# Optimization experiments

Hardware: AMD Instinct MI355X
Metric: run time of the kernel (lower is better)

## Reference

```python
import jax, jax.numpy as jnp
import numpy as np
from itertools import product

S0 = 384          # voxel grid size per max_data_size
N0 = 500_000      # active surface voxels
NF_IN, NF = 2, 16
EPS = 1e-4        # scn.BatchNormReLU default eps


def _make_nbr(lin, S, offs):
    # submanifold rulebook: nbr[k, i] = row of active neighbor of site i at offset k, else sentinel N
    N = len(lin)
    x = lin // (S * S); y = (lin // S) % S; z = lin % S
    nbr = np.full((len(offs), N), N, np.int32)
    for k, (dx, dy, dz) in enumerate(offs):
        nx, ny, nz = x + dx, y + dy, z + dz
        valid = (nx >= 0) & (nx < S) & (ny >= 0) & (ny < S) & (nz >= 0) & (nz < S)
        q = (nx * S + ny) * S + nz
        pos = np.minimum(np.searchsorted(lin, q), N - 1)
        nbr[k] = np.where(valid & (lin[pos] == q), pos, N).astype(np.int32)
    return nbr


def _downsample(lin, S):
    # half-resolution active sites, unpool parent map, and 2x2x2 stride-2 conv rulebook
    x = lin // (S * S); y = (lin // S) % S; z = lin % S
    Sh = S // 2
    plin = ((x // 2) * Sh + (y // 2)) * Sh + (z // 2)
    lin_h = np.unique(plin)
    parent = np.searchsorted(lin_h, plin).astype(np.int32)
    xh = lin_h // (Sh * Sh); yh = (lin_h // Sh) % Sh; zh = lin_h % Sh
    N, Nh = len(lin), len(lin_h)
    down = np.full((8, Nh), N, np.int32)
    for k, (ox, oy, oz) in enumerate(product((0, 1), repeat=3)):
        q = ((2 * xh + ox) * S + (2 * yh + oy)) * S + (2 * zh + oz)
        pos = np.minimum(np.searchsorted(lin, q), N - 1)
        down[k] = np.where(lin[pos] == q, pos, N).astype(np.int32)
    return lin_h, parent, down


def setup_inputs() -> dict:
    rng = np.random.default_rng(0)
    cand = rng.integers(0, S0 ** 3, size=int(N0 * 1.1))
    lin0 = np.unique(cand)[:N0]
    assert len(lin0) == N0
    offs27 = list(product((-1, 0, 1), repeat=3))
    nbr0 = _make_nbr(lin0, S0, offs27)
    lin1, parent01, down01 = _downsample(lin0, S0)
    nbr1 = _make_nbr(lin1, S0 // 2, offs27)
    lin2, parent12, down12 = _downsample(lin1, S0 // 2)
    nbr2 = _make_nbr(lin2, S0 // 4, offs27)

    key = jax.random.key(0)
    ks = jax.random.split(key, 16)
    n = lambda k, sh, sc: jax.random.normal(k, sh, jnp.float32) * sc
    return dict(
        feats=n(ks[0], (N0, NF_IN), 1.0),
        w_p1=n(ks[1], (27, NF_IN, NF), 1.0 / np.sqrt(27 * NF_IN)),
        blk_bn1_g=1.0 + n(ks[2], (3, NF), 0.1), blk_bn1_b=n(ks[3], (3, NF), 0.1),
        blk_w1=n(ks[4], (3, 27, NF, NF), 1.0 / np.sqrt(27 * NF)),
        blk_bn2_g=1.0 + n(ks[5], (3, NF), 0.1), blk_bn2_b=n(ks[6], (3, NF), 0.1),
        blk_w2=n(ks[7], (3, 27, NF, NF), 1.0 / np.sqrt(27 * NF)),
        down_bn_g=1.0 + n(ks[8], (2, NF), 0.1), down_bn_b=n(ks[9], (2, NF), 0.1),
        down_w=n(ks[10], (2, 8, NF, NF), 1.0 / np.sqrt(8 * NF)),
        bn3_g=1.0 + n(ks[11], (3 * NF,), 0.1), bn3_b=n(ks[12], (3 * NF,), 0.1),
        w_sdf=n(ks[13], (3 * NF, 1), 1.0 / np.sqrt(3 * NF)),
        b_sdf=jnp.zeros((1,), jnp.float32),
        nbr0=jnp.asarray(nbr0), nbr1=jnp.asarray(nbr1), nbr2=jnp.asarray(nbr2),
        down01=jnp.asarray(down01), down12=jnp.asarray(down12),
        parent01=jnp.asarray(parent01), parent12=jnp.asarray(parent12),
    )


def _sconv(x, nbr, W):
    # rulebook gather-GEMM-accumulate sparse conv.
    # x: [Nin, Cin], nbr: [K, Nout] (index Nin == inactive sentinel), W: [K, Cin, Cout]
    xp = jnp.concatenate([x, jnp.zeros((1, x.shape[1]), x.dtype)], 0)
    acc0 = jnp.zeros((nbr.shape[1], W.shape[2]), x.dtype)
    def step(acc, kw):
        idx, Wk = kw
        return acc + xp[idx] @ Wk, None
    out, _ = jax.lax.scan(step, acc0, (nbr, W))
    return out


def _bnrelu(x, g, b):
    # SCN BatchNorm: batch stats over active sites only
    m = x.mean(0); v = x.var(0)
    return jax.nn.relu((x - m) * jax.lax.rsqrt(v + EPS) * g + b)


def _res_block(x, nbr, g1, b1, w1, g2, b2, w2):
    # pre-activation residual block, identity skip (in == out channels)
    h = _sconv(_bnrelu(x, g1, b1), nbr, w1)
    h = _sconv(_bnrelu(h, g2, b2), nbr, w2)
    return x + h


def reference(feats, w_p1, blk_bn1_g, blk_bn1_b, blk_w1, blk_bn2_g, blk_bn2_b,
              blk_w2, down_bn_g, down_bn_b, down_w, bn3_g, bn3_b, w_sdf, b_sdf,
              nbr0, nbr1, nbr2, down01, down12, parent01, parent12):
    blk = lambda x, nbr, i: _res_block(x, nbr, blk_bn1_g[i], blk_bn1_b[i], blk_w1[i],
                                       blk_bn2_g[i], blk_bn2_b[i], blk_w2[i])
    x = _sconv(feats, nbr0, w_p1)                                    # p1: submanifold conv nf_in->nf
    r0 = blk(x, nbr0, 0)                                             # FCN level 0 block
    y1 = _sconv(_bnrelu(r0, down_bn_g[0], down_bn_b[0]), down01, down_w[0])  # stride-2 conv
    r1 = blk(y1, nbr1, 1)                                            # level 1 block
    z2 = _sconv(_bnrelu(r1, down_bn_g[1], down_bn_b[1]), down12, down_w[1])
    r2 = blk(z2, nbr2, 2)                                            # level 2 block
    j1 = jnp.concatenate([r1, r2[parent12]], axis=-1)                # UnPool + JoinTable -> 2*nf
    j0 = jnp.concatenate([r0, j1[parent01]], axis=-1)                # UnPool + JoinTable -> 3*nf
    h = _bnrelu(j0, bn3_g, bn3_b)                                    # p3
    return h @ w_sdf + b_sdf                                         # sdf linear, [N0, 1]
```

## Files before the change

### kernel.cpp

```cpp
#include <hip/hip_runtime.h>

#define BN_EPS 1e-4f
#define NREP 8

typedef _Float16 f16x8 __attribute__((ext_vector_type(8)));
typedef _Float16 f16x4 __attribute__((ext_vector_type(4)));
typedef _Float16 f16x2 __attribute__((ext_vector_type(2)));
typedef float f32x4 __attribute__((ext_vector_type(4)));

__global__ __launch_bounds__(256) void tr_k(const int* __restrict__ nbr,
                                            int* __restrict__ nbrT,
                                            int N, int Nin)
{
    const int i = blockIdx.x * 256 + threadIdx.x;
    if (i >= N) return;
    int v[32];
#pragma unroll
    for (int k = 0; k < 27; ++k) v[k] = nbr[(size_t)k * N + i];
#pragma unroll
    for (int k = 27; k < 32; ++k) v[k] = Nin;
    int4* dst = (int4*)(nbrT + (size_t)i * 32);
#pragma unroll
    for (int j = 0; j < 8; ++j)
        dst[j] = make_int4(v[4 * j], v[4 * j + 1], v[4 * j + 2], v[4 * j + 3]);
}

__global__ __launch_bounds__(256, 4) void conv16t_k(
    const _Float16* __restrict__ A16,
    const int* __restrict__ nbrT,
    const _Float16* __restrict__ WB,
    float* __restrict__ out,
    float* __restrict__ stats_out,
    int Nout, int Nin, int addSkip)
{
    constexpr int K = 27, PAIRS = 14;
    __shared__ int lds[4][16 * 36];
    const int wave = threadIdx.x >> 6, lane = threadIdx.x & 63;
    const int l15 = lane & 15, q = lane >> 4;
    const int h = q & 1;
    const int th = q >> 1;
    int* L = lds[wave];

    f16x8 bfr[PAIRS];
#pragma unroll
    for (int p = 0; p < PAIRS; ++p)
        bfr[p] = *(const f16x8*)(WB + ((size_t)p * 64 + lane) * 8);

    const int ngroups = (Nout + 15) >> 4;
    float s = 0.f, ss = 0.f;

    for (int grp = blockIdx.x * 4 + wave; grp < ngroups; grp += gridDim.x * 4) {
        const int base = grp * 16;
        const int site = min(base + l15, Nout - 1);

        const int4* src = (const int4*)(nbrT + (size_t)site * 32);
        const int4 c0 = src[q];
        const int4 c1 = src[q + 4];
        *(int4*)(L + l15 * 36 + q * 4) = c0;
        *(int4*)(L + l15 * 36 + 16 + q * 4) = c1;

        int idxs[PAIRS];
#pragma unroll
        for (int p = 0; p < PAIRS; ++p) {
            const int t = 2 * p + ((2 * p + 1 < K) ? th : 0);
            idxs[p] = L[l15 * 36 + t];
        }

        f32x4 acc0 = {0.f, 0.f, 0.f, 0.f}, acc1 = {0.f, 0.f, 0.f, 0.f};
#pragma unroll
        for (int p = 0; p < PAIRS; ++p) {
            const int idx = idxs[p];
            if (__any(idx < Nin)) {
                f16x8 a = {};
                if (idx < Nin)
                    a = *(const f16x8*)(A16 + (size_t)idx * 16 + h * 8);
                if (p & 1) acc1 = __builtin_amdgcn_mfma_f32_16x16x32_f16(a, bfr[p], acc1, 0, 0, 0);
                else       acc0 = __builtin_amdgcn_mfma_f32_16x16x32_f16(a, bfr[p], acc0, 0, 0, 0);
            }
        }

#pragma unroll
        for (int r = 0; r < 4; ++r) {
            const int row = base + q * 4 + r;
            float v = acc0[r] + acc1[r];
            if (row < Nout) {
                float* op = out + (size_t)row * 16 + l15;
                if (addSkip) v += *op;
                *op = v;
                s += v; ss += v * v;
            }
        }
    }

    if (stats_out) {
        s  += __shfl_xor(s, 16);  s  += __shfl_xor(s, 32);
        ss += __shfl_xor(ss, 16); ss += __shfl_xor(ss, 32);
        __shared__ float red[4][32];
        if (lane < 16) { red[wave][l15] = s; red[wave][16 + l15] = ss; }
        __syncthreads();
        if (threadIdx.x < 32) {
            const int t2 = threadIdx.x;
            float* bank = stats_out + (blockIdx.x & (NREP - 1)) * 128;
            atomicAdd(bank + (t2 < 16 ? t2 : 48 + t2),
                      red[0][t2] + red[1][t2] + red[2][t2] + red[3][t2]);
        }
    }
}

template <int K>
__global__ __launch_bounds__(256, 4) void conv16_k(
    const _Float16* __restrict__ A16, const int* __restrict__ nbr,
    const _Float16* __restrict__ WB, float* __restrict__ out,
    float* __restrict__ stats_out, int Nout, int Nin, int addSkip)
{
    constexpr int PAIRS = (K + 1) / 2;
    const int wave = threadIdx.x >> 6, lane = threadIdx.x & 63;
    const int l15 = lane & 15, q = lane >> 4;
    const int h = q & 1, th = q >> 1;

    f16x8 bfr[PAIRS];
#pragma unroll
    for (int p = 0; p < PAIRS; ++p)
        bfr[p] = *(const f16x8*)(WB + ((size_t)p * 64 + lane) * 8);

    const int ngroups = (Nout + 15) >> 4;
    float s = 0.f, ss = 0.f;

    for (int grp = blockIdx.x * 4 + wave; grp < ngroups; grp += gridDim.x * 4) {
        const int base = grp * 16;
        const int site = min(base + l15, Nout - 1);
        f32x4 acc0 = {0.f, 0.f, 0.f, 0.f}, acc1 = {0.f, 0.f, 0.f, 0.f};
#pragma unroll
        for (int p = 0; p < PAIRS; ++p) {
            const int t = 2 * p + ((2 * p + 1 < K) ? th : 0);
            const int idx = nbr[(size_t)t * Nout + site];
            f16x8 a = {};
            if (idx < Nin)
                a = *(const f16x8*)(A16 + (size_t)idx * 16 + h * 8);
            if (p & 1) acc1 = __builtin_amdgcn_mfma_f32_16x16x32_f16(a, bfr[p], acc1, 0, 0, 0);
            else       acc0 = __builtin_amdgcn_mfma_f32_16x16x32_f16(a, bfr[p], acc0, 0, 0, 0);
        }
#pragma unroll
        for (int r = 0; r < 4; ++r) {
            const int row = base + q * 4 + r;
            float v = acc0[r] + acc1[r];
            if (row < Nout) {
                float* op = out + (size_t)row * 16 + l15;
                if (addSkip) v += *op;
                *op = v;
                s += v; ss += v * v;
            }
        }
    }

    if (stats_out) {
        s  += __shfl_xor(s, 16);  s  += __shfl_xor(s, 32);
        ss += __shfl_xor(ss, 16); ss += __shfl_xor(ss, 32);
        __shared__ float red[4][32];
        if (lane < 16) { red[wave][l15] = s; red[wave][16 + l15] = ss; }
        __syncthreads();
        if (threadIdx.x < 32) {
            const int t2 = threadIdx.x;
            float* bank = stats_out + (blockIdx.x & (NREP - 1)) * 128;
            atomicAdd(bank + (t2 < 16 ? t2 : 48 + t2),
                      red[0][t2] + red[1][t2] + red[2][t2] + red[3][t2]);
        }
    }
}

__global__ __launch_bounds__(256, 4) void convp1t_k(
    const _Float16* __restrict__ F16,
    const int* __restrict__ nbrT,
    const _Float16* __restrict__ WB,
    float* __restrict__ out, float* __restrict__ stats_out, int Nout)
{
    __shared__ int lds[4][16 * 36];
    const int wave = threadIdx.x >> 6, lane = threadIdx.x & 63;
    const int l15 = lane & 15, q = lane >> 4;
    int* L = lds[wave];

    f16x8 b0 = *(const f16x8*)(WB + (size_t)lane * 8);
    f16x8 b1 = *(const f16x8*)(WB + ((size_t)64 + lane) * 8);

    const int ngroups = (Nout + 15) >> 4;
    float s = 0.f, ss = 0.f;

    for (int grp = blockIdx.x * 4 + wave; grp < ngroups; grp += gridDim.x * 4) {
        const int base = grp * 16;
        const int site = min(base + l15, Nout - 1);

        const int4* src = (const int4*)(nbrT + (size_t)site * 32);
        const int4 c0 = src[q];
        const int4 c1 = src[q + 4];
        *(int4*)(L + l15 * 36 + q * 4) = c0;
        *(int4*)(L + l15 * 36 + 16 + q * 4) = c1;

        f32x4 acc = {0.f, 0.f, 0.f, 0.f};
#pragma unroll
        for (int mf = 0; mf < 2; ++mf) {
            int tid[4];
#pragma unroll
            for (int jt = 0; jt < 4; ++jt)
                tid[jt] = L[l15 * 36 + mf * 16 + q * 4 + jt];
            f16x8 a;
#pragma unroll
            for (int jt = 0; jt < 4; ++jt) {
                const int idx = tid[jt];
                f16x2 f = {};
                if (idx < Nout)
                    f = *(const f16x2*)(F16 + (size_t)idx * 2);
                a[jt * 2] = f.x; a[jt * 2 + 1] = f.y;
            }
            acc = __builtin_amdgcn_mfma_f32_16x16x32_f16(a, mf ? b1 : b0, acc, 0, 0, 0);
        }
#pragma unroll
        for (int r = 0; r < 4; ++r) {
            const int row = base + q * 4 + r;
            const float v = acc[r];
            if (row < Nout) {
                out[(size_t)row * 16 + l15] = v;
                s += v; ss += v * v;
            }
        }
    }

    s  += __shfl_xor(s, 16);  s  += __shfl_xor(s, 32);
    ss += __shfl_xor(ss, 16); ss += __shfl_xor(ss, 32);
    __shared__ float red[4][32];
    if (lane < 16) { red[wave][l15] = s; red[wave][16 + l15] = ss; }
    __syncthreads();
    if (threadIdx.x < 32) {
        const int t2 = threadIdx.x;
        float* bank = stats_out + (blockIdx.x & (NREP - 1)) * 128;
        atomicAdd(bank + (t2 < 16 ? t2 : 48 + t2),
                  red[0][t2] + red[1][t2] + red[2][t2] + red[3][t2]);
    }
}

__global__ void pack_k(const float* __restrict__ w_p1, const float* __restrict__ w1,
                       const float* __restrict__ w2, const float* __restrict__ dw,
                       _Float16* __restrict__ WBp1, _Float16* __restrict__ WB27,
                       _Float16* __restrict__ WB8)
{
    const int b = blockIdx.x;
    if (b == 0) {
        for (int v = threadIdx.x; v < 2 * 64 * 8; v += 256) {
            const int mf = v >> 9, lane = (v >> 3) & 63, j = v & 7;
            const int qq = lane >> 4, n = lane & 15;
            const int kg = mf * 32 + qq * 8 + j;
            const int t = kg >> 1, cin = kg & 1;
            WBp1[v] = (t < 27) ? (_Float16)w_p1[t * 32 + cin * 16 + n] : (_Float16)0.f;
        }
    } else if (b <= 6) {
        const int ti = b - 1, lvl = ti >> 1;
        const float* src = ((ti & 1) ? w2 : w1) + lvl * 6912;
        _Float16* dst = WB27 + (size_t)ti * (14 * 64 * 8);
        for (int v = threadIdx.x; v < 14 * 64 * 8; v += 256) {
            const int p = v >> 9, lane = (v >> 3) & 63, j = v & 7;
            const int qq = lane >> 4, n = lane & 15;
            const int t = 2 * p + (qq >> 1);
            const int cin = (qq & 1) * 8 + j;
            dst[v] = (t < 27) ? (_Float16)src[t * 256 + cin * 16 + n] : (_Float16)0.f;
        }
    } else {
        const int ti = b - 7;
        const float* src = dw + ti * 2048;
        _Float16* dst = WB8 + (size_t)ti * (4 * 64 * 8);
        for (int v = threadIdx.x; v < 4 * 64 * 8; v += 256) {
            const int p = v >> 9, lane = (v >> 3) & 63, j = v & 7;
            const int qq = lane >> 4, n = lane & 15;
            const int t = 2 * p + (qq >> 1);
            const int cin = (qq & 1) * 8 + j;
            dst[v] = (_Float16)src[t * 256 + cin * 16 + n];
        }
    }
}

__global__ __launch_bounds__(256) void apply16_k(
    const float* __restrict__ x, const float* __restrict__ stats,
    const float* __restrict__ g, const float* __restrict__ b,
    _Float16* __restrict__ A16, int N, float invN)
{
    const int t = blockIdx.x * 256 + threadIdx.x;
    if (t >= (N + 1) * 4) return;
    const int n = t >> 2, c = (t & 3) * 4;
    f16x4 r;
    if (n == N) {
        r[0] = r[1] = r[2] = r[3] = (_Float16)0.f;
    } else {
        const float4 v = *(const float4*)(x + (size_t)n * 16 + c);
        float vv[4] = {v.x, v.y, v.z, v.w};
#pragma unroll
        for (int i = 0; i < 4; ++i) {
            float su = 0.f, sq = 0.f;
#pragma unroll
            for (int rep = 0; rep < NREP; ++rep) {
                su += stats[rep * 128 + c + i];
                sq += stats[rep * 128 + 64 + c + i];
            }
            const float mean = su * invN;
            const float var  = sq * invN - mean * mean;
            const float sc   = g[c + i] * rsqrtf(var + BN_EPS);
            const float bi   = fmaf(-mean, sc, b[c + i]);
            r[i] = (_Float16)fmaxf(fmaf(vv[i], sc, bi), 0.f);
        }
    }
    *(f16x4*)(A16 + (size_t)n * 16 + c) = r;
}

__global__ void f16cvt_k(const float* __restrict__ f, _Float16* __restrict__ F16, int N)
{
    const int t = blockIdx.x * 256 + threadIdx.x;
    if (t > N) return;
    f16x2 r;
    if (t == N) { r[0] = r[1] = (_Float16)0.f; }
    else { const float2 v = *(const float2*)(f + (size_t)t * 2); r[0] = (_Float16)v.x; r[1] = (_Float16)v.y; }
    *(f16x2*)(F16 + (size_t)t * 2) = r;
}

__global__ void fin_k(float* __restrict__ stats, const float* __restrict__ g,
                      const float* __restrict__ b, float* __restrict__ sb,
                      int C, float invN)
{
    const int c = threadIdx.x;
    if (c < C) {
        float su = 0.f, sq = 0.f;
#pragma unroll
        for (int rep = 0; rep < NREP; ++rep) {
            su += stats[rep * 128 + c];
            sq += stats[rep * 128 + 64 + c];
        }
        const float mean = su * invN;
        const float var = sq * invN - mean * mean;
        const float s = g[c] * rsqrtf(var + BN_EPS);
        sb[c] = s;
        sb[64 + c] = fmaf(-mean, s, b[c]);
    }
}

__device__ __forceinline__ float wred(float v) {
#pragma unroll
    for (int off = 32; off > 0; off >>= 1) v += __shfl_xor(v, off);
    return v;
}

__global__ __launch_bounds__(256) void gstats_k(
    const float* __restrict__ R0, const float* __restrict__ R1,
    const float* __restrict__ R2, const int* __restrict__ p01,
    const int* __restrict__ p12, float* __restrict__ stats, int N0)
{
    float s[48], q[48];
#pragma unroll
    for (int c = 0; c < 48; ++c) { s[c] = 0.f; q[c] = 0.f; }

    for (int n = blockIdx.x * blockDim.x + threadIdx.x; n < N0;
         n += gridDim.x * blockDim.x) {
        const int i1 = p01[n];
        const int i2 = p12[i1];
        const float4* a0 = (const float4*)(R0 + (size_t)n * 16);
        const float4* a1 = (const float4*)(R1 + (size_t)i1 * 16);
        const float4* a2 = (const float4*)(R2 + (size_t)i2 * 16);
#pragma unroll
        for (int j = 0; j < 4; ++j) {
            const float4 v = a0[j]; const int c = 4 * j;
            s[c] += v.x; q[c] += v.x * v.x; s[c+1] += v.y; q[c+1] += v.y * v.y;
            s[c+2] += v.z; q[c+2] += v.z * v.z; s[c+3] += v.w; q[c+3] += v.w * v.w;
        }
#pragma unroll
        for (int j = 0; j < 4; ++j) {
            const float4 v = a1[j]; const int c = 16 + 4 * j;
            s[c] += v.x; q[c] += v.x * v.x; s[c+1] += v.y; q[c+1] += v.y * v.y;
            s[c+2] += v.z; q[c+2] += v.z * v.z; s[c+3] += v.w; q[c+3] += v.w * v.w;
        }
#pragma unroll
        for (int j = 0; j < 4; ++j) {
            const float4 v = a2[j]; const int c = 32 + 4 * j;
            s[c] += v.x; q[c] += v.x * v.x; s[c+1] += v.y; q[c+1] += v.y * v.y;
            s[c+2] += v.z; q[c+2] += v.z * v.z; s[c+3] += v.w; q[c+3] += v.w * v.w;
        }
    }

    __shared__ float red[4][96];
    const int wave = threadIdx.x >> 6, lane = threadIdx.x & 63;
#pragma unroll
    for (int c = 0; c < 48; ++c) {
        const float ss = wred(s[c]);
        const float qq = wred(q[c]);
        if (lane == 0) { red[wave][c] = ss; red[wave][48 + c] = qq; }
    }
    __syncthreads();
    const int t = threadIdx.x;
    if (t < 96) {
        float* bank = stats + (blockIdx.x & (NREP - 1)) * 128;
        const float v = red[0][t] + red[1][t] + red[2][t] + red[3][t];
        atomicAdd(bank + (t < 48 ? t : 64 + (t - 48)), v);
    }
}

__global__ __launch_bounds__(256) void out_k(
    const float* __restrict__ R0, const float* __restrict__ R1,
    const float* __restrict__ R2, const int* __restrict__ p01,
    const int* __restrict__ p12, const float* __restrict__ sb,
    const float* __restrict__ wsdf, const float* __restrict__ bsdf,
    float* __restrict__ out, int N0)
{
    const int n = blockIdx.x * 256 + threadIdx.x;
    if (n >= N0) return;
    const int i1 = p01[n];
    const int i2 = p12[i1];
    float acc = bsdf[0];
    const float4* a0 = (const float4*)(R0 + (size_t)n * 16);
    const float4* a1 = (const float4*)(R1 + (size_t)i1 * 16);
    const float4* a2 = (const float4*)(R2 + (size_t)i2 * 16);
#pragma unroll
    for (int j = 0; j < 4; ++j) {
        const float4 v = a0[j]; const int c = 4 * j;
        acc += fmaxf(fmaf(v.x, sb[c+0], sb[64+c+0]), 0.f) * wsdf[c+0];
        acc += fmaxf(fmaf(v.y, sb[c+1], sb[64+c+1]), 0.f) * wsdf[c+1];
        acc += fmaxf(fmaf(v.z, sb[c+2], sb[64+c+2]), 0.f) * wsdf[c+2];
        acc += fmaxf(fmaf(v.w, sb[c+3], sb[64+c+3]), 0.f) * wsdf[c+3];
    }
#pragma unroll
    for (int j = 0; j < 4; ++j) {
        const float4 v = a1[j]; const int c = 16 + 4 * j;
        acc += fmaxf(fmaf(v.x, sb[c+0], sb[64+c+0]), 0.f) * wsdf[c+0];
        acc += fmaxf(fmaf(v.y, sb[c+1], sb[64+c+1]), 0.f) * wsdf[c+1];
        acc += fmaxf(fmaf(v.z, sb[c+2], sb[64+c+2]), 0.f) * wsdf[c+2];
        acc += fmaxf(fmaf(v.w, sb[c+3], sb[64+c+3]), 0.f) * wsdf[c+3];
    }
#pragma unroll
    for (int j = 0; j < 4; ++j) {
        const float4 v = a2[j]; const int c = 32 + 4 * j;
        acc += fmaxf(fmaf(v.x, sb[c+0], sb[64+c+0]), 0.f) * wsdf[c+0];
        acc += fmaxf(fmaf(v.y, sb[c+1], sb[64+c+1]), 0.f) * wsdf[c+1];
        acc += fmaxf(fmaf(v.z, sb[c+2], sb[64+c+2]), 0.f) * wsdf[c+2];
        acc += fmaxf(fmaf(v.w, sb[c+3], sb[64+c+3]), 0.f) * wsdf[c+3];
    }
    out[n] = acc;
}

extern "C" void kernel_launch(void* const* d_in, const int* in_sizes, int n_in,
                              void* d_out, int out_size, void* d_ws, size_t ws_size,
                              hipStream_t stream)
{
    const float* feats = (const float*)d_in[0];
    const float* w_p1  = (const float*)d_in[1];
    const float* bn1g  = (const float*)d_in[2];
    const float* bn1b  = (const float*)d_in[3];
    const float* w1    = (const float*)d_in[4];
    const float* bn2g  = (const float*)d_in[5];
    const float* bn2b  = (const float*)d_in[6];
    const float* w2    = (const float*)d_in[7];
    const float* dbng  = (const float*)d_in[8];
    const float* dbnb  = (const float*)d_in[9];
    const float* dw    = (const float*)d_in[10];
    const float* bn3g  = (const float*)d_in[11];
    const float* bn3b  = (const float*)d_in[12];
    const float* wsdf  = (const float*)d_in[13];
    const float* bsdf  = (const float*)d_in[14];
    const int* nbr0    = (const int*)d_in[15];
    const int* nbr1    = (const int*)d_in[16];
    const int* nbr2    = (const int*)d_in[17];
    const int* down01  = (const int*)d_in[18];
    const int* down12  = (const int*)d_in[19];
    const int* p01     = (const int*)d_in[20];
    const int* p12     = (const int*)d_in[21];

    const int N0 = in_sizes[0] / 2;
    const int N1 = in_sizes[18] / 8;
    const int N2 = in_sizes[19] / 8;

    char* wp = (char*)d_ws;
    auto alloc = [&](size_t bytes) { char* r = wp; wp += (bytes + 255) & ~(size_t)255; return r; };
    float* T  = (float*)alloc((size_t)N0 * 16 * 4);
    float* R0 = (float*)alloc((size_t)N0 * 16 * 4);
    float* R1 = (float*)alloc((size_t)N1 * 16 * 4);
    float* R2 = (float*)alloc((size_t)N2 * 16 * 4);
    float* st = (float*)alloc(9 * NREP * 128 * 4);
    float* sb = (float*)alloc(128 * 4);
    _Float16* A16  = (_Float16*)alloc((size_t)(N0 + 1) * 16 * 2);
    _Float16* F16  = (_Float16*)alloc((size_t)(N0 + 1) * 2 * 2);
    _Float16* WBp1 = (_Float16*)alloc(2 * 64 * 8 * 2);
    _Float16* WB27 = (_Float16*)alloc(6 * 14 * 64 * 8 * 2);
    _Float16* WB8  = (_Float16*)alloc(2 * 4 * 64 * 8 * 2);
    int* nbrT = (int*)alloc((size_t)N0 * 32 * 4);

    hipMemsetAsync(st, 0, 9 * NREP * 128 * sizeof(float), stream);

    const dim3 B(256);
    auto cgrid = [](int n) {
        const int g = (((n + 15) / 16) + 3) / 4;
        return dim3((unsigned)(g < 2048 ? g : 2048));
    };
    auto agrid = [](int n) { return dim3((unsigned)(((n + 1) * 4 + 255) / 256)); };
    auto lgrid = [](int n) { return dim3((unsigned)((n + 255) / 256)); };
    const float i0 = 1.0f / N0, i1 = 1.0f / N1, i2 = 1.0f / N2;
    auto S = [&](int i) { return st + i * NREP * 128; };
    auto W27 = [&](int i) { return WB27 + (size_t)i * (14 * 64 * 8); };
    auto W8  = [&](int i) { return WB8 + (size_t)i * (4 * 64 * 8); };

    pack_k<<<9, B, 0, stream>>>(w_p1, w1, w2, dw, WBp1, WB27, WB8);
    f16cvt_k<<<lgrid(N0 + 1), B, 0, stream>>>(feats, F16, N0);

    tr_k<<<lgrid(N0), B, 0, stream>>>(nbr0, nbrT, N0, N0);
    convp1t_k<<<cgrid(N0), B, 0, stream>>>(F16, nbrT, WBp1, R0, S(0), N0);
    apply16_k<<<agrid(N0), B, 0, stream>>>(R0, S(0), bn1g, bn1b, A16, N0, i0);
    conv16t_k<<<cgrid(N0), B, 0, stream>>>(A16, nbrT, W27(0), T, S(1), N0, N0, 0);
    apply16_k<<<agrid(N0), B, 0, stream>>>(T, S(1), bn2g, bn2b, A16, N0, i0);
    conv16t_k<<<cgrid(N0), B, 0, stream>>>(A16, nbrT, W27(1), R0, S(2), N0, N0, 1);
    apply16_k<<<agrid(N0), B, 0, stream>>>(R0, S(2), dbng, dbnb, A16, N0, i0);
    conv16_k<8><<<cgrid(N1), B, 0, stream>>>(A16, down01, W8(0), R1, S(3), N1, N0, 0);

    tr_k<<<lgrid(N1), B, 0, stream>>>(nbr1, nbrT, N1, N1);
    apply16_k<<<agrid(N1), B, 0, stream>>>(R1, S(3), bn1g + 16, bn1b + 16, A16, N1, i1);
    conv16t_k<<<cgrid(N1), B, 0, stream>>>(A16, nbrT, W27(2), T, S(4), N1, N1, 0);
    apply16_k<<<agrid(N1), B, 0, stream>>>(T, S(4), bn2g + 16, bn2b + 16, A16, N1, i1);
    conv16t_k<<<cgrid(N1), B, 0, stream>>>(A16, nbrT, W27(3), R1, S(5), N1, N1, 1);
    apply16_k<<<agrid(N1), B, 0, stream>>>(R1, S(5), dbng + 16, dbnb + 16, A16, N1, i1);
    conv16_k<8><<<cgrid(N2), B, 0, stream>>>(A16, down12, W8(1), R2, S(6), N2, N1, 0);

    tr_k<<<lgrid(N2), B, 0, stream>>>(nbr2, nbrT, N2, N2);
    apply16_k<<<agrid(N2), B, 0, stream>>>(R2, S(6), bn1g + 32, bn1b + 32, A16, N2, i2);
    conv16t_k<<<cgrid(N2), B, 0, stream>>>(A16, nbrT, W27(4), T, S(7), N2, N2, 0);
    apply16_k<<<agrid(N2), B, 0, stream>>>(T, S(7), bn2g + 32, bn2b + 32, A16, N2, i2);
    conv16t_k<<<cgrid(N2), B, 0, stream>>>(A16, nbrT, W27(5), R2, nullptr, N2, N2, 1);

    gstats_k<<<512, B, 0, stream>>>(R0, R1, R2, p01, p12, S(8), N0);
    fin_k<<<1, 64, 0, stream>>>(S(8), bn3g, bn3b, sb, 48, i0);
    out_k<<<lgrid(N0), B, 0, stream>>>(R0, R1, R2, p01, p12, sb, wsdf, bsdf,
                                       (float*)d_out, N0);
}
```

Baseline: 789.1 us.

## Stage conv weights in LDS, prefetch rulebook rows, and vectorize output writes

The 27-tap conv kernel now copies its packed weights into shared memory once per block and reads them from there instead of holding 14 fragments in registers. It prefetches the next group's neighbor indices during the current group's work, and routes accumulators through an LDS transpose so each lane writes and reads the skip input with float4 accesses. Per-channel stats are reduced with shuffles across lanes, and the number of atomic banks and the grid cap are both doubled. The intent is lower register pressure, coalesced stores and less atomic contention, at the cost of extra LDS traffic and LDS weight reads on every MFMA.

```diff
diff --git a/kernel.cpp b/kernel.cpp
--- a/kernel.cpp
+++ b/kernel.cpp
@@ -1,7 +1,7 @@
 #include <hip/hip_runtime.h>
 
 #define BN_EPS 1e-4f
-#define NREP 8
+#define NREP 16
 
 typedef _Float16 f16x8 __attribute__((ext_vector_type(8)));
 typedef _Float16 f16x4 __attribute__((ext_vector_type(4)));
@@ -34,36 +34,58 @@
     int Nout, int Nin, int addSkip)
 {
     constexpr int K = 27, PAIRS = 14;
-    __shared__ int lds[4][16 * 36];
+    __shared__ _Float16 WBs[PAIRS * 64 * 8];
+    __shared__ int IDX[4][16 * 36];
+    __shared__ float TRS[4][16 * 20];
+    __shared__ float RED[4][32];
+
     const int wave = threadIdx.x >> 6, lane = threadIdx.x & 63;
     const int l15 = lane & 15, q = lane >> 4;
-    const int h = q & 1;
-    const int th = q >> 1;
-    int* L = lds[wave];
-
-    f16x8 bfr[PAIRS];
-#pragma unroll
-    for (int p = 0; p < PAIRS; ++p)
-        bfr[p] = *(const f16x8*)(WB + ((size_t)p * 64 + lane) * 8);
+    const int h = q & 1, th = q >> 1;
+    int* L = IDX[wave];
+    float* Tr = TRS[wave];
+
+    {
+        const float4* src = (const float4*)WB;
+        float4* dst = (float4*)WBs;
+        for (int v = threadIdx.x; v < PAIRS * 64; v += 256) dst[v] = src[v];
+    }
+    __syncthreads();
 
     const int ngroups = (Nout + 15) >> 4;
-    float s = 0.f, ss = 0.f;
-
-    for (int grp = blockIdx.x * 4 + wave; grp < ngroups; grp += gridDim.x * 4) {
+    const int stride = gridDim.x * 4;
+    const int rr = lane >> 2, cc = (lane & 3) * 4;
+    float sj[4] = {0.f, 0.f, 0.f, 0.f}, qj[4] = {0.f, 0.f, 0.f, 0.f};
+
+    int grp = blockIdx.x * 4 + wave;
+    int4 c0, c1;
+    if (grp < ngroups) {
+        const int site = min(grp * 16 + l15, Nout - 1);
+        const int4* src = (const int4*)(nbrT + (size_t)site * 32);
+        c0 = src[q]; c1 = src[q + 4];
+    }
+
+    while (grp < ngroups) {
         const int base = grp * 16;
-        const int site = min(base + l15, Nout - 1);
-
-        const int4* src = (const int4*)(nbrT + (size_t)site * 32);
-        const int4 c0 = src[q];
-        const int4 c1 = src[q + 4];
+
         *(int4*)(L + l15 * 36 + q * 4) = c0;
         *(int4*)(L + l15 * 36 + 16 + q * 4) = c1;
 
+        const int srow = base + rr;
+        float4 skip = make_float4(0.f, 0.f, 0.f, 0.f);
+        if (addSkip && srow < Nout)
+            skip = *(const float4*)(out + (size_t)srow * 16 + cc);
+
         int idxs[PAIRS];
 #pragma unroll
-        for (int p = 0; p < PAIRS; ++p) {
-            const int t = 2 * p + ((2 * p + 1 < K) ? th : 0);
-            idxs[p] = L[l15 * 36 + t];
+        for (int p = 0; p < PAIRS; ++p)
+            idxs[p] = L[l15 * 36 + 2 * p + ((2 * p + 1 < K) ? th : 0)];
+
+        const int gn = grp + stride;
+        if (gn < ngroups) {
+            const int nsite = min(gn * 16 + l15, Nout - 1);
+            const int4* nsrc = (const int4*)(nbrT + (size_t)nsite * 32);
+            c0 = nsrc[q]; c1 = nsrc[q + 4];
         }
 
         f32x4 acc0 = {0.f, 0.f, 0.f, 0.f}, acc1 = {0.f, 0.f, 0.f, 0.f};
@@ -74,35 +96,52 @@
                 f16x8 a = {};
                 if (idx < Nin)
                     a = *(const f16x8*)(A16 + (size_t)idx * 16 + h * 8);
-                if (p & 1) acc1 = __builtin_amdgcn_mfma_f32_16x16x32_f16(a, bfr[p], acc1, 0, 0, 0);
-                else       acc0 = __builtin_amdgcn_mfma_f32_16x16x32_f16(a, bfr[p], acc0, 0, 0, 0);
-            }
-        }
-
-#pragma unroll
-        for (int r = 0; r < 4; ++r) {
-            const int row = base + q * 4 + r;
-            float v = acc0[r] + acc1[r];
-            if (row < Nout) {
-                float* op = out + (size_t)row * 16 + l15;
-                if (addSkip) v += *op;
-                *op = v;
-                s += v; ss += v * v;
-            }
-        }
+                const f16x8 b = *(const f16x8*)(WBs + ((size_t)p * 64 + lane) * 8);
+                if (p & 1) acc1 = __builtin_amdgcn_mfma_f32_16x16x32_f16(a, b, acc1, 0, 0, 0);
+                else       acc0 = __builtin_amdgcn_mfma_f32_16x16x32_f16(a, b, acc0, 0, 0, 0);
+            }
+        }
+
+#pragma unroll
+        for (int r = 0; r < 4; ++r)
+            Tr[(q * 4 + r) * 20 + l15] = acc0[r] + acc1[r];
+        float4 v4;
+        v4.x = Tr[rr * 20 + cc + 0] + skip.x;
+        v4.y = Tr[rr * 20 + cc + 1] + skip.y;
+        v4.z = Tr[rr * 20 + cc + 2] + skip.z;
+        v4.w = Tr[rr * 20 + cc + 3] + skip.w;
+        if (srow < Nout) {
+            *(float4*)(out + (size_t)srow * 16 + cc) = v4;
+            sj[0] += v4.x; qj[0] += v4.x * v4.x;
+            sj[1] += v4.y; qj[1] += v4.y * v4.y;
+            sj[2] += v4.z; qj[2] += v4.z * v4.z;
+            sj[3] += v4.w; qj[3] += v4.w * v4.w;
+        }
+        grp = gn;
     }
 
     if (stats_out) {
-        s  += __shfl_xor(s, 16);  s  += __shfl_xor(s, 32);
-        ss += __shfl_xor(ss, 16); ss += __shfl_xor(ss, 32);
-        __shared__ float red[4][32];
-        if (lane < 16) { red[wave][l15] = s; red[wave][16 + l15] = ss; }
+#pragma unroll
+        for (int m = 4; m < 64; m <<= 1) {
+#pragma unroll
+            for (int j = 0; j < 4; ++j) {
+                sj[j] += __shfl_xor(sj[j], m);
+                qj[j] += __shfl_xor(qj[j], m);
+            }
+        }
+        if (lane < 4) {
+#pragma unroll
+            for (int j = 0; j < 4; ++j) {
+                RED[wave][lane * 4 + j] = sj[j];
+                RED[wave][16 + lane * 4 + j] = qj[j];
+            }
+        }
         __syncthreads();
         if (threadIdx.x < 32) {
             const int t2 = threadIdx.x;
             float* bank = stats_out + (blockIdx.x & (NREP - 1)) * 128;
             atomicAdd(bank + (t2 < 16 ? t2 : 48 + t2),
-                      red[0][t2] + red[1][t2] + red[2][t2] + red[3][t2]);
+                      RED[0][t2] + RED[1][t2] + RED[2][t2] + RED[3][t2]);
         }
     }
 }
@@ -490,7 +529,7 @@
     const dim3 B(256);
     auto cgrid = [](int n) {
         const int g = (((n + 15) / 16) + 3) / 4;
-        return dim3((unsigned)(g < 2048 ? g : 2048));
+        return dim3((unsigned)(g < 4096 ? g : 4096));
     };
     auto agrid = [](int n) { return dim3((unsigned)(((n + 1) * 4 + 255) / 256)); };
     auto lgrid = [](int n) { return dim3((unsigned)((n + 255) / 256)); };
```

New measurement: 885.2 us. 1.12x slower.
